# Kernel tuning notes

Measured on AMD Instinct MI355X. Metric: run time of the kernel, lower is better.

The kernel has to match this reference:

```python
import jax, jax.numpy as jnp
from jax import lax
import numpy as np

B, S, H, E = 512, 128, 512, 128
VEC_FEAT = 128
WORD_VOCABS = [1000, 500, 200]
GOAL_VOCAB = 32000
TACTIC_VOCAB = 1024
NUM_ENC_LAYERS = 3  # -> 2 extra encoder linear layers


def setup_inputs() -> dict:
    key = jax.random.key(0)
    ks = iter(jax.random.split(key, 32))
    s = 0.05
    inp = {}
    inp["vec_features"] = jax.random.normal(next(ks), (B, VEC_FEAT), dtype=jnp.float32)
    inp["word_features"] = jax.random.randint(next(ks), (B, len(WORD_VOCABS)), 0, 200)
    inp["goals"] = jax.random.randint(next(ks), (B, S), 0, GOAL_VOCAB)
    # word feature embedding tables (distinct vocab sizes)
    inp["wemb0"] = jax.random.normal(next(ks), (WORD_VOCABS[0], E), dtype=jnp.float32) * s
    inp["wemb1"] = jax.random.normal(next(ks), (WORD_VOCABS[1], E), dtype=jnp.float32) * s
    inp["wemb2"] = jax.random.normal(next(ks), (WORD_VOCABS[2], E), dtype=jnp.float32) * s
    # features_in: Linear(vec_feat + 3*E -> H), torch convention W [out, in]
    inp["feat_in_W"] = jax.random.normal(next(ks), (H, VEC_FEAT + len(WORD_VOCABS) * E), dtype=jnp.float32) * s
    inp["feat_in_b"] = jnp.zeros((H,), dtype=jnp.float32)
    # stacked encoder layers: (L-1) x Linear(H -> H)
    inp["enc_W"] = jax.random.normal(next(ks), (NUM_ENC_LAYERS - 1, H, H), dtype=jnp.float32) * s
    inp["enc_b"] = jnp.zeros((NUM_ENC_LAYERS - 1, H), dtype=jnp.float32)
    inp["goal_emb"] = jax.random.normal(next(ks), (GOAL_VOCAB, H), dtype=jnp.float32) * s
    # GRU weights, torch layout: [3H, H] with gate order (r, z, n)
    inp["gru_Wih"] = jax.random.normal(next(ks), (3 * H, H), dtype=jnp.float32) * s
    inp["gru_Whh"] = jax.random.normal(next(ks), (3 * H, H), dtype=jnp.float32) * s
    inp["gru_bih"] = jnp.zeros((3 * H,), dtype=jnp.float32)
    inp["gru_bhh"] = jnp.zeros((3 * H,), dtype=jnp.float32)
    inp["dec_in_W"] = jax.random.normal(next(ks), (H, 2 * H), dtype=jnp.float32) * s
    inp["dec_in_b"] = jnp.zeros((H,), dtype=jnp.float32)
    inp["dec_out_W"] = jax.random.normal(next(ks), (TACTIC_VOCAB, H), dtype=jnp.float32) * s
    inp["dec_out_b"] = jnp.zeros((TACTIC_VOCAB,), dtype=jnp.float32)
    return inp


def reference(vec_features, word_features, goals, wemb0, wemb1, wemb2,
              feat_in_W, feat_in_b, enc_W, enc_b, goal_emb,
              gru_Wih, gru_Whh, gru_bih, gru_bhh,
              dec_in_W, dec_in_b, dec_out_W, dec_out_b):
    batch = vec_features.shape[0]
    h = gru_Whh.shape[1]
    # Goal GRU branch: relu(embedding) per token, then GRU recurrence.
    x_seq = jax.nn.relu(goal_emb[goals])                    # [B, S, H]
    # Precompute input-side gate projections for all timesteps: [B, S, 3H]
    gi = jnp.einsum('bsh,gh->bsg', x_seq, gru_Wih) + gru_bih

    def step(hid, gi_t):
        gh = hid @ gru_Whh.T + gru_bhh                      # [B, 3H]
        i_r, i_z, i_n = jnp.split(gi_t, 3, axis=-1)
        h_r, h_z, h_n = jnp.split(gh, 3, axis=-1)
        r = jax.nn.sigmoid(i_r + h_r)
        z = jax.nn.sigmoid(i_z + h_z)
        n = jnp.tanh(i_n + r * h_n)
        new = (1.0 - z) * n + z * hid
        return new, None

    h0 = jnp.zeros((batch, h), dtype=x_seq.dtype)
    goal_data, _ = lax.scan(step, h0, jnp.swapaxes(gi, 0, 1))  # [B, H]

    # Features branch: word-feature embeddings + vec features -> MLP
    embs = [wemb0[word_features[:, 0]], wemb1[word_features[:, 1]], wemb2[word_features[:, 2]]]
    feats = jnp.concatenate([vec_features] + embs, axis=1)
    features_data = feats @ feat_in_W.T + feat_in_b
    for i in range(enc_W.shape[0]):
        features_data = jax.nn.relu(features_data) @ enc_W[i].T + enc_b[i]

    full = jax.nn.relu(jnp.concatenate([goal_data, features_data], axis=1))
    full = jax.nn.relu(full @ dec_in_W.T + dec_in_b)
    logits = full @ dec_out_W.T + dec_out_b
    return jax.nn.log_softmax(logits, axis=1)
```

## Files before the change

### kernel.cpp

```cpp
#include <hip/hip_runtime.h>
#include <hip/hip_bf16.h>

typedef unsigned short ushort_t;
typedef __attribute__((ext_vector_type(8))) short short8;
typedef __attribute__((ext_vector_type(4))) float f32x4;
typedef __attribute__((ext_vector_type(4))) int i32x4;

__device__ __forceinline__ ushort_t f2bf(float f) {
    unsigned x = __builtin_bit_cast(unsigned, f);
    unsigned r = x + 0x7fffu + ((x >> 16) & 1u);
    return (ushort_t)(r >> 16);
}
__device__ __forceinline__ float bf2f(ushort_t u) {
    return __builtin_bit_cast(float, ((unsigned)u) << 16);
}

__device__ __forceinline__ void store16_cc(void* p, i32x4 v) {
    asm volatile("global_store_dwordx4 %0, %1, off sc0 sc1" :: "v"(p), "v"(v) : "memory");
}
__device__ __forceinline__ i32x4 load16_cc(const void* p) {
    i32x4 r;
    asm volatile("global_load_dwordx4 %0, %1, off sc0 sc1" : "=v"(r) : "v"(p));
    return r;
}
__device__ __forceinline__ unsigned load_u16_raw(const ushort_t* p) {
    unsigned r;
    asm volatile("global_load_ushort %0, %1, off" : "=v"(r) : "v"(p));
    return r;
}

template<bool RELU>
__global__ void k_conv(const float* __restrict__ src, ushort_t* __restrict__ dst, int n) {
    int i = (blockIdx.x * blockDim.x + threadIdx.x) * 4;
    int stride = gridDim.x * blockDim.x * 4;
    for (; i < n; i += stride) {
        float4 v = *(const float4*)(src + i);
        if (RELU) {
            v.x = fmaxf(v.x, 0.f); v.y = fmaxf(v.y, 0.f);
            v.z = fmaxf(v.z, 0.f); v.w = fmaxf(v.w, 0.f);
        }
        dst[i + 0] = f2bf(v.x); dst[i + 1] = f2bf(v.y);
        dst[i + 2] = f2bf(v.z); dst[i + 3] = f2bf(v.w);
    }
}

__global__ void k_whh_frag(const float* __restrict__ whh, ushort_t* __restrict__ out) {
    int idx = blockIdx.x * blockDim.x + threadIdx.x;
    if (idx >= 16 * 6 * 16 * 64 * 8) return;
    int e  = idx & 7;
    int s  = idx >> 3;
    int l  = s & 63;
    int s2 = s >> 6;
    int kk = s2 & 15;
    int s3 = s2 >> 4;
    int f  = s3 % 6;
    int j  = s3 / 6;
    int ng = (f >> 1) * 512 + j * 32 + (f & 1) * 16 + (l & 15);
    int k  = kk * 32 + ((l >> 4) << 3) + e;
    out[idx] = f2bf(whh[(size_t)ng * 512 + k]);
}

__global__ void k_feats(const float* __restrict__ vec, const int* __restrict__ wf,
                        const float* __restrict__ w0, const float* __restrict__ w1,
                        const float* __restrict__ w2, ushort_t* __restrict__ out) {
    int idx = blockIdx.x * blockDim.x + threadIdx.x;
    if (idx >= 512 * 512) return;
    int b = idx >> 9, k = idx & 511;
    float v;
    if (k < 128)       v = vec[b * 128 + k];
    else if (k < 256)  v = w0[wf[b * 3 + 0] * 128 + (k - 128)];
    else if (k < 384)  v = w1[wf[b * 3 + 1] * 128 + (k - 256)];
    else               v = w2[wf[b * 3 + 2] * 128 + (k - 384)];
    out[idx] = f2bf(v);
}

template<bool RELU, bool OUTBF>
__global__ __launch_bounds__(256) void k_gemm(const ushort_t* __restrict__ A,
                                              const ushort_t* __restrict__ W,
                                              const float* __restrict__ bias,
                                              void* __restrict__ Cout,
                                              int M, int N, int K) {
    __shared__ __attribute__((aligned(16))) ushort_t As[128 * 64];
    __shared__ __attribute__((aligned(16))) ushort_t Ws[128 * 64];
    const int tid = threadIdx.x;
    const int lane = tid & 63, w = tid >> 6;
    const int wm = w >> 1, wn = w & 1;
    const int m0 = blockIdx.y * 128, n0 = blockIdx.x * 128;
    const int l16 = lane & 15, lq = lane >> 4;
    f32x4 acc[4][4] = {};

    for (int k0 = 0; k0 < K; k0 += 64) {
        #pragma unroll
        for (int c = 0; c < 4; ++c) {
            int chunk = w * 4 + c;
            int d = chunk * 1024 + lane * 16;
            int row = d >> 7;
            int dlin = d ^ ((row & 7) << 4);
            int col = (dlin & 127) >> 1;
            const ushort_t* ga = A + (size_t)(m0 + row) * K + k0 + col;
            __builtin_amdgcn_global_load_lds(
                (const __attribute__((address_space(1))) void*)ga,
                (__attribute__((address_space(3))) void*)(((char*)As) + chunk * 1024),
                16, 0, 0);
        }
        #pragma unroll
        for (int c = 0; c < 4; ++c) {
            int chunk = w * 4 + c;
            int d = chunk * 1024 + lane * 16;
            int row = d >> 7;
            int dlin = d ^ ((row & 7) << 4);
            int col = (dlin & 127) >> 1;
            const ushort_t* gw = W + (size_t)(n0 + row) * K + k0 + col;
            __builtin_amdgcn_global_load_lds(
                (const __attribute__((address_space(1))) void*)gw,
                (__attribute__((address_space(3))) void*)(((char*)Ws) + chunk * 1024),
                16, 0, 0);
        }
        asm volatile("s_waitcnt vmcnt(0)" ::: "memory");
        __syncthreads();

        #pragma unroll
        for (int kk = 0; kk < 2; ++kk) {
            short8 af[4], bfr[4];
            #pragma unroll
            for (int m = 0; m < 4; ++m) {
                int row = wm * 64 + m * 16 + l16;
                int addr = (row * 128 + kk * 64 + lq * 16) ^ ((row & 7) << 4);
                af[m] = *(const short8*)((const char*)As + addr);
            }
            #pragma unroll
            for (int n = 0; n < 4; ++n) {
                int row = wn * 64 + n * 16 + l16;
                int addr = (row * 128 + kk * 64 + lq * 16) ^ ((row & 7) << 4);
                bfr[n] = *(const short8*)((const char*)Ws + addr);
            }
            #pragma unroll
            for (int m = 0; m < 4; ++m)
                #pragma unroll
                for (int n = 0; n < 4; ++n)
                    acc[m][n] = __builtin_amdgcn_mfma_f32_16x16x32_bf16(af[m], bfr[n], acc[m][n], 0, 0, 0);
        }
        __syncthreads();
    }

    #pragma unroll
    for (int m = 0; m < 4; ++m) {
        int row = m0 + wm * 64 + m * 16 + lq * 4;
        #pragma unroll
        for (int n = 0; n < 4; ++n) {
            int col = n0 + wn * 64 + n * 16 + l16;
            float bv = bias[col];
            #pragma unroll
            for (int r = 0; r < 4; ++r) {
                float v = acc[m][n][r] + bv;
                if (RELU) v = fmaxf(v, 0.f);
                if (OUTBF) ((ushort_t*)Cout)[(size_t)(row + r) * N + col] = f2bf(v);
                else       ((float*)Cout)[(size_t)(row + r) * N + col] = v;
            }
        }
    }
}

__global__ __launch_bounds__(128) void k_recur(const ushort_t* __restrict__ G,
                                               const ushort_t* __restrict__ WhhF,
                                               const int* __restrict__ goals,
                                               const float* __restrict__ bhh,
                                               ushort_t* __restrict__ Hx,
                                               int* __restrict__ flags,
                                               float* __restrict__ goal_out) {
    __shared__ __attribute__((aligned(16))) ushort_t Bs[6 * 16 * 64 * 8];
    __shared__ __attribute__((aligned(16))) ushort_t Hs[32 * 32];
    __shared__ __attribute__((aligned(16))) int Tk[32 * 128];
    const int bid = blockIdx.x;
    const int rg = bid & 15;
    const int cg = bid >> 4;
    const int r0 = rg * 32, c0 = cg * 32;
    const int tid = threadIdx.x, lane = tid & 63, w = tid >> 6;
    const int l16 = lane & 15, lq = lane >> 4;

    {
        const ushort_t* src = WhhF + (size_t)cg * 49152;
        for (int c = 0; c < 48; ++c) {
            int chunk = w * 48 + c;
            __builtin_amdgcn_global_load_lds(
                (const __attribute__((address_space(1))) void*)(src + chunk * 512 + lane * 8),
                (__attribute__((address_space(3))) void*)(((char*)Bs) + chunk * 1024),
                16, 0, 0);
        }
        const int* tsrc = goals + r0 * 128;
        for (int c = 0; c < 8; ++c) {
            int chunk = w * 8 + c;
            __builtin_amdgcn_global_load_lds(
                (const __attribute__((address_space(1))) void*)(tsrc + chunk * 256 + lane * 4),
                (__attribute__((address_space(3))) void*)(((char*)Tk) + chunk * 1024),
                16, 0, 0);
        }
        asm volatile("s_waitcnt vmcnt(0)" ::: "memory");
        __syncthreads();
    }

    const int rowbase = r0 + w * 16;
    const int lrow = w * 16 + lq * 4;
    float hst[2][4];
    #pragma unroll
    for (int q = 0; q < 2; ++q)
        #pragma unroll
        for (int r = 0; r < 4; ++r) hst[q][r] = 0.f;

    float bh[3][2];
    #pragma unroll
    for (int g = 0; g < 3; ++g)
        #pragma unroll
        for (int q = 0; q < 2; ++q) bh[g][q] = bhh[g * 512 + c0 + q * 16 + l16];

    float gc[3][4][2];
    #pragma unroll
    for (int r = 0; r < 4; ++r) {
        int tok = Tk[(lrow + r) * 128];
        const ushort_t* gr = G + (size_t)tok * 1536;
        #pragma unroll
        for (int q = 0; q < 2; ++q) {
            int cl = c0 + q * 16 + l16;
            gc[0][r][q] = bf2f(gr[cl]);
            gc[1][r][q] = bf2f(gr[512 + cl]);
            gc[2][r][q] = bf2f(gr[1024 + cl]);
        }
    }

    unsigned gn[3][4][2];
    auto issueGN = [&](int tn) {
        #pragma unroll
        for (int r = 0; r < 4; ++r) {
            int tok = Tk[(lrow + r) * 128 + tn];
            const ushort_t* gr = G + (size_t)tok * 1536;
            #pragma unroll
            for (int q = 0; q < 2; ++q) {
                int cl = c0 + q * 16 + l16;
                gn[0][r][q] = load_u16_raw(gr + cl);
                gn[1][r][q] = load_u16_raw(gr + 512 + cl);
                gn[2][r][q] = load_u16_raw(gr + 1024 + cl);
            }
        }
    };

    for (int t = 0; t < 128; ++t) {
        const int tn = (t < 127) ? t + 1 : 127;
        f32x4 acc[6] = {};
        if (t) {
            const ushort_t* hb = Hx + ((size_t)(t & 1) << 18);
            short8 af[16];
            #pragma unroll
            for (int kk = 0; kk < 16; ++kk) {
                const ushort_t* pa = hb + (size_t)(rowbase + l16) * 512 + kk * 32 + lq * 8;
                af[kk] = __builtin_bit_cast(short8, load16_cc(pa));
            }
            issueGN(tn);
            asm volatile("s_waitcnt vmcnt(24)" ::: "memory");
            __builtin_amdgcn_sched_barrier(0);
            #pragma unroll
            for (int kk = 0; kk < 16; ++kk) {
                #pragma unroll
                for (int f = 0; f < 6; ++f) {
                    short8 bfr = *(const short8*)((const char*)Bs + ((f * 16 + kk) * 64 + lane) * 16);
                    acc[f] = __builtin_amdgcn_mfma_f32_16x16x32_bf16(af[kk], bfr, acc[f], 0, 0, 0);
                }
            }
        } else {
            issueGN(tn);
        }

        #pragma unroll
        for (int r = 0; r < 4; ++r) {
            #pragma unroll
            for (int q = 0; q < 2; ++q) {
                float ir = gc[0][r][q], iz = gc[1][r][q], in_ = gc[2][r][q];
                float hr = acc[q][r] + bh[0][q];
                float hz = acc[2 + q][r] + bh[1][q];
                float hn = acc[4 + q][r] + bh[2][q];
                float rr = 1.f / (1.f + __expf(-(ir + hr)));
                float zz = 1.f / (1.f + __expf(-(iz + hz)));
                float x = in_ + rr * hn;
                float ax = fabsf(x);
                float th = 1.f - 2.f / (__expf(2.f * ax) + 1.f);
                th = copysignf(th, x);
                float hnew = (1.f - zz) * th + zz * hst[q][r];
                hst[q][r] = hnew;
                Hs[(w * 16 + lq * 4 + r) * 32 + q * 16 + l16] = f2bf(hnew);
            }
        }
        __syncthreads();

        {
            int row = tid >> 2, coff = (tid & 3) * 8;
            i32x4 v = *(const i32x4*)&Hs[row * 32 + coff];
            ushort_t* ho = Hx + ((size_t)((t + 1) & 1) << 18)
                         + (size_t)(r0 + row) * 512 + c0 + coff;
            store16_cc(ho, v);
        }
        asm volatile("s_waitcnt vmcnt(0)" ::: "memory");
        __builtin_amdgcn_sched_barrier(0);
        __syncthreads();

        if (tid == 0)
            __hip_atomic_store(&flags[bid], t + 1, __ATOMIC_RELAXED, __HIP_MEMORY_SCOPE_AGENT);
        if (tid < 16) {
            int* pf = &flags[(tid << 4) | rg];
            for (int it = 0; it < 100000; ++it) {
                if (__hip_atomic_load(pf, __ATOMIC_RELAXED, __HIP_MEMORY_SCOPE_AGENT) >= t + 1)
                    break;
                __builtin_amdgcn_s_sleep(1);
            }
        }
        __syncthreads();

        #pragma unroll
        for (int g = 0; g < 3; ++g)
            #pragma unroll
            for (int r = 0; r < 4; ++r)
                #pragma unroll
                for (int q = 0; q < 2; ++q)
                    gc[g][r][q] = bf2f((ushort_t)gn[g][r][q]);
    }

    #pragma unroll
    for (int r = 0; r < 4; ++r) {
        int brow = rowbase + lq * 4 + r;
        #pragma unroll
        for (int q = 0; q < 2; ++q) {
            int cl = c0 + q * 16 + l16;
            goal_out[(size_t)brow * 512 + cl] = hst[q][r];
        }
    }
}

__global__ void k_concat(const float* __restrict__ gd, const ushort_t* __restrict__ r2,
                         ushort_t* __restrict__ out) {
    int idx = blockIdx.x * blockDim.x + threadIdx.x;
    if (idx >= 512 * 1024) return;
    int b = idx >> 10, c = idx & 1023;
    out[idx] = (c < 512) ? f2bf(fmaxf(gd[b * 512 + c], 0.f)) : r2[b * 512 + (c - 512)];
}

__global__ __launch_bounds__(256) void k_lsm(float* __restrict__ logits) {
    __shared__ float sm[4];
    __shared__ float ss[4];
    float* p = logits + (size_t)blockIdx.x * 1024;
    int tid = threadIdx.x;
    float4 v = ((const float4*)p)[tid];
    float m = fmaxf(fmaxf(v.x, v.y), fmaxf(v.z, v.w));
    #pragma unroll
    for (int o = 32; o >= 1; o >>= 1) m = fmaxf(m, __shfl_xor(m, o));
    if ((tid & 63) == 0) sm[tid >> 6] = m;
    __syncthreads();
    m = fmaxf(fmaxf(sm[0], sm[1]), fmaxf(sm[2], sm[3]));
    float s = __expf(v.x - m) + __expf(v.y - m) + __expf(v.z - m) + __expf(v.w - m);
    #pragma unroll
    for (int o = 32; o >= 1; o >>= 1) s += __shfl_xor(s, o);
    if ((tid & 63) == 0) ss[tid >> 6] = s;
    __syncthreads();
    s = ss[0] + ss[1] + ss[2] + ss[3];
    float lse = m + logf(s);
    v.x -= lse; v.y -= lse; v.z -= lse; v.w -= lse;
    ((float4*)p)[tid] = v;
}

static constexpr size_t OFF_G     = 0;
static constexpr size_t OFF_AREL  = OFF_G     + 98304000ull;
static constexpr size_t OFF_WIH   = OFF_AREL  + 32768000ull;
static constexpr size_t OFF_WHHF  = OFF_WIH   + 1572864ull;
static constexpr size_t OFF_HX    = OFF_WHHF  + 1572864ull;
static constexpr size_t OFF_FLAGS = OFF_HX    + 1048576ull;
static constexpr size_t OFF_GOAL  = OFF_FLAGS + 1024ull;
static constexpr size_t OFF_FEATS = OFF_GOAL  + 1048576ull;
static constexpr size_t OFF_W0    = OFF_FEATS + 524288ull;
static constexpr size_t OFF_W12   = OFF_W0    + 524288ull;
static constexpr size_t OFF_R0    = OFF_W12   + 1048576ull;
static constexpr size_t OFF_R1    = OFF_R0    + 524288ull;
static constexpr size_t OFF_R2    = OFF_R1    + 524288ull;
static constexpr size_t OFF_DECA  = OFF_R2    + 524288ull;
static constexpr size_t OFF_WD1   = OFF_DECA  + 1048576ull;
static constexpr size_t OFF_D1    = OFF_WD1   + 1048576ull;
static constexpr size_t OFF_WD2   = OFF_D1    + 524288ull;
static constexpr size_t WS_NEED   = OFF_WD2   + 1048576ull;

extern "C" void kernel_launch(void* const* d_in, const int* in_sizes, int n_in,
                              void* d_out, int out_size, void* d_ws, size_t ws_size,
                              hipStream_t stream) {
    if (ws_size < WS_NEED) return;

    const float* vec   = (const float*)d_in[0];
    const int*   wf    = (const int*)d_in[1];
    const int*   goals = (const int*)d_in[2];
    const float* we0   = (const float*)d_in[3];
    const float* we1   = (const float*)d_in[4];
    const float* we2   = (const float*)d_in[5];
    const float* fiW   = (const float*)d_in[6];
    const float* fib   = (const float*)d_in[7];
    const float* encW  = (const float*)d_in[8];
    const float* encb  = (const float*)d_in[9];
    const float* gemb  = (const float*)d_in[10];
    const float* Wih   = (const float*)d_in[11];
    const float* Whh   = (const float*)d_in[12];
    const float* bih   = (const float*)d_in[13];
    const float* bhh   = (const float*)d_in[14];
    const float* diW   = (const float*)d_in[15];
    const float* dib   = (const float*)d_in[16];
    const float* doW   = (const float*)d_in[17];
    const float* dob   = (const float*)d_in[18];

    char* ws = (char*)d_ws;
    ushort_t* G_     = (ushort_t*)(ws + OFF_G);
    ushort_t* Arel   = (ushort_t*)(ws + OFF_AREL);
    ushort_t* WihB   = (ushort_t*)(ws + OFF_WIH);
    ushort_t* WhhF   = (ushort_t*)(ws + OFF_WHHF);
    ushort_t* Hx     = (ushort_t*)(ws + OFF_HX);
    int*      flags  = (int*)(ws + OFF_FLAGS);
    float*    goalD  = (float*)(ws + OFF_GOAL);
    ushort_t* featsA = (ushort_t*)(ws + OFF_FEATS);
    ushort_t* W0     = (ushort_t*)(ws + OFF_W0);
    ushort_t* W1     = (ushort_t*)(ws + OFF_W12);
    ushort_t* W2     = W1 + 262144;
    ushort_t* R0     = (ushort_t*)(ws + OFF_R0);
    ushort_t* R1     = (ushort_t*)(ws + OFF_R1);
    ushort_t* R2     = (ushort_t*)(ws + OFF_R2);
    ushort_t* DecA   = (ushort_t*)(ws + OFF_DECA);
    ushort_t* Wd1    = (ushort_t*)(ws + OFF_WD1);
    ushort_t* D1     = (ushort_t*)(ws + OFF_D1);
    ushort_t* Wd2    = (ushort_t*)(ws + OFF_WD2);

    hipMemsetAsync(ws + OFF_FLAGS, 0, 1024, stream);

    auto cgrid = [](int n) { int b = (n / 4 + 255) / 256; return b > 2048 ? 2048 : b; };
    k_conv<false><<<cgrid(786432),  256, 0, stream>>>(Wih,  WihB, 786432);
    k_conv<false><<<cgrid(262144),  256, 0, stream>>>(fiW,  W0,   262144);
    k_conv<false><<<cgrid(524288),  256, 0, stream>>>(encW, W1,   524288);
    k_conv<false><<<cgrid(524288),  256, 0, stream>>>(diW,  Wd1,  524288);
    k_conv<false><<<cgrid(524288),  256, 0, stream>>>(doW,  Wd2,  524288);
    k_conv<true ><<<2048,           256, 0, stream>>>(gemb, Arel, 16384000);
    k_whh_frag<<<3072, 256, 0, stream>>>(Whh, WhhF);
    k_feats<<<1024, 256, 0, stream>>>(vec, wf, we0, we1, we2, featsA);

    k_gemm<false, true><<<dim3(12, 250), 256, 0, stream>>>(Arel, WihB, bih, G_, 32000, 1536, 512);

    k_gemm<true, true><<<dim3(4, 4), 256, 0, stream>>>(featsA, W0, fib,        R0, 512, 512, 512);
    k_gemm<true, true><<<dim3(4, 4), 256, 0, stream>>>(R0,     W1, encb,       R1, 512, 512, 512);
    k_gemm<true, true><<<dim3(4, 4), 256, 0, stream>>>(R1,     W2, encb + 512, R2, 512, 512, 512);

    {
        const ushort_t* Gc = G_; const ushort_t* Wc = WhhF;
        const int* gc = goals; const float* bc = bhh;
        ushort_t* hx = Hx; int* fl = flags; float* go = goalD;
        void* kargs[] = { &Gc, &Wc, &gc, &bc, &hx, &fl, &go };
        hipLaunchCooperativeKernel((const void*)k_recur, dim3(256), dim3(128),
                                   kargs, 0, stream);
    }

    k_concat<<<2048, 256, 0, stream>>>(goalD, R2, DecA);
    k_gemm<true,  true ><<<dim3(4, 4), 256, 0, stream>>>(DecA, Wd1, dib, D1, 512, 512, 1024);
    k_gemm<false, false><<<dim3(8, 4), 256, 0, stream>>>(D1, Wd2, dob, (float*)d_out, 512, 1024, 512);
    k_lsm<<<512, 256, 0, stream>>>((float*)d_out);
}
```

Baseline: 1.173 ms.

## Replace block-wide flag barrier with per-chunk readiness polling in GRU recurrence

The persistent GRU kernel no longer waits for all 16 peer blocks to publish their hidden-state slice before each step. Each wave starts with its own slice from LDS, then polls the peer flags and loads and multiplies each 32-column chunk as soon as its producer has signalled, double-buffering the A fragments. One __syncthreads per step is also dropped, and the gate-input prefetch is reissued at the end of each step rather than kept in a separate register copy. This targets the grid-wide barrier cost on the sequential recurrence, at the price of frequent uncached flag loads, more control flow, and correctness that depends on memory ordering between the flag store and the data store.

```diff
diff --git a/kernel.cpp b/kernel.cpp
--- a/kernel.cpp
+++ b/kernel.cpp
@@ -213,22 +213,8 @@
         #pragma unroll
         for (int q = 0; q < 2; ++q) bh[g][q] = bhh[g * 512 + c0 + q * 16 + l16];
 
-    float gc[3][4][2];
-    #pragma unroll
-    for (int r = 0; r < 4; ++r) {
-        int tok = Tk[(lrow + r) * 128];
-        const ushort_t* gr = G + (size_t)tok * 1536;
-        #pragma unroll
-        for (int q = 0; q < 2; ++q) {
-            int cl = c0 + q * 16 + l16;
-            gc[0][r][q] = bf2f(gr[cl]);
-            gc[1][r][q] = bf2f(gr[512 + cl]);
-            gc[2][r][q] = bf2f(gr[1024 + cl]);
-        }
-    }
-
-    unsigned gn[3][4][2];
-    auto issueGN = [&](int tn) {
+    unsigned gv[3][4][2];
+    auto issueGV = [&](int tn) {
         #pragma unroll
         for (int r = 0; r < 4; ++r) {
             int tok = Tk[(lrow + r) * 128 + tn];
@@ -236,44 +222,83 @@
             #pragma unroll
             for (int q = 0; q < 2; ++q) {
                 int cl = c0 + q * 16 + l16;
-                gn[0][r][q] = load_u16_raw(gr + cl);
-                gn[1][r][q] = load_u16_raw(gr + 512 + cl);
-                gn[2][r][q] = load_u16_raw(gr + 1024 + cl);
+                gv[0][r][q] = load_u16_raw(gr + cl);
+                gv[1][r][q] = load_u16_raw(gr + 512 + cl);
+                gv[2][r][q] = load_u16_raw(gr + 1024 + cl);
             }
         }
     };
-
+    issueGV(0);
+
+    int* fp = flags + (((lane & 15) << 4) | rg);
+
+    f32x4 acc[6];
     for (int t = 0; t < 128; ++t) {
-        const int tn = (t < 127) ? t + 1 : 127;
-        f32x4 acc[6] = {};
+        #pragma unroll
+        for (int f = 0; f < 6; ++f) acc[f] = (f32x4){0.f, 0.f, 0.f, 0.f};
+
+        auto domfma = [&](short8 af, int kk) {
+            #pragma unroll
+            for (int f = 0; f < 6; ++f) {
+                short8 bfr = *(const short8*)((const char*)Bs + ((f * 16 + kk) * 64 + lane) * 16);
+                acc[f] = __builtin_amdgcn_mfma_f32_16x16x32_bf16(af, bfr, acc[f], 0, 0, 0);
+            }
+        };
+        auto pollrdy = [&]() -> unsigned {
+            int v;
+            asm volatile("global_load_dword %0, %1, off sc0 sc1" : "=v"(v) : "v"(fp));
+            asm volatile("s_waitcnt vmcnt(0)" ::: "memory");
+            __builtin_amdgcn_sched_barrier(0);
+            return (unsigned)(__ballot(v >= t) & 0xffffull);
+        };
+
         if (t) {
             const ushort_t* hb = Hx + ((size_t)(t & 1) << 18);
-            short8 af[16];
-            #pragma unroll
-            for (int kk = 0; kk < 16; ++kk) {
-                const ushort_t* pa = hb + (size_t)(rowbase + l16) * 512 + kk * 32 + lq * 8;
-                af[kk] = __builtin_bit_cast(short8, load16_cc(pa));
-            }
-            issueGN(tn);
-            asm volatile("s_waitcnt vmcnt(24)" ::: "memory");
+            auto tadr = [&](int j) {
+                return hb + (size_t)(rowbase + l16) * 512 + j * 32 + lq * 8;
+            };
+            short8 own = *(const short8*)&Hs[(w * 16 + l16) * 32 + lq * 8];
+            domfma(own, cg);
+            unsigned rdy = pollrdy();
+            short8 afr[2];
+            {
+                int j1 = (cg + 1) & 15;
+                int guard = 0;
+                while (!((rdy >> j1) & 1)) {
+                    rdy = pollrdy();
+                    if (++guard > 200000) break;
+                }
+                afr[1] = __builtin_bit_cast(short8, load16_cc(tadr(j1)));
+            }
+            #pragma unroll
+            for (int s = 1; s <= 15; ++s) {
+                if (s < 15) {
+                    int jn = (cg + s + 1) & 15;
+                    int guard = 0;
+                    while (!((rdy >> jn) & 1)) {
+                        rdy = pollrdy();
+                        if (++guard > 200000) break;
+                    }
+                    afr[(s + 1) & 1] = __builtin_bit_cast(short8, load16_cc(tadr(jn)));
+                    asm volatile("s_waitcnt vmcnt(1)" ::: "memory");
+                } else {
+                    asm volatile("s_waitcnt vmcnt(0)" ::: "memory");
+                }
+                __builtin_amdgcn_sched_barrier(0);
+                domfma(afr[s & 1], (cg + s) & 15);
+            }
+        } else {
+            asm volatile("s_waitcnt vmcnt(0)" ::: "memory");
             __builtin_amdgcn_sched_barrier(0);
-            #pragma unroll
-            for (int kk = 0; kk < 16; ++kk) {
-                #pragma unroll
-                for (int f = 0; f < 6; ++f) {
-                    short8 bfr = *(const short8*)((const char*)Bs + ((f * 16 + kk) * 64 + lane) * 16);
-                    acc[f] = __builtin_amdgcn_mfma_f32_16x16x32_bf16(af[kk], bfr, acc[f], 0, 0, 0);
-                }
-            }
-        } else {
-            issueGN(tn);
         }
 
         #pragma unroll
         for (int r = 0; r < 4; ++r) {
             #pragma unroll
             for (int q = 0; q < 2; ++q) {
-                float ir = gc[0][r][q], iz = gc[1][r][q], in_ = gc[2][r][q];
+                float ir = bf2f((ushort_t)gv[0][r][q]);
+                float iz = bf2f((ushort_t)gv[1][r][q]);
+                float in_ = bf2f((ushort_t)gv[2][r][q]);
                 float hr = acc[q][r] + bh[0][q];
                 float hz = acc[2 + q][r] + bh[1][q];
                 float hn = acc[4 + q][r] + bh[2][q];
@@ -288,7 +313,6 @@
                 Hs[(w * 16 + lq * 4 + r) * 32 + q * 16 + l16] = f2bf(hnew);
             }
         }
-        __syncthreads();
 
         {
             int row = tid >> 2, coff = (tid & 3) * 8;
@@ -301,25 +325,12 @@
         __builtin_amdgcn_sched_barrier(0);
         __syncthreads();
 
-        if (tid == 0)
-            __hip_atomic_store(&flags[bid], t + 1, __ATOMIC_RELAXED, __HIP_MEMORY_SCOPE_AGENT);
-        if (tid < 16) {
-            int* pf = &flags[(tid << 4) | rg];
-            for (int it = 0; it < 100000; ++it) {
-                if (__hip_atomic_load(pf, __ATOMIC_RELAXED, __HIP_MEMORY_SCOPE_AGENT) >= t + 1)
-                    break;
-                __builtin_amdgcn_s_sleep(1);
-            }
-        }
-        __syncthreads();
-
-        #pragma unroll
-        for (int g = 0; g < 3; ++g)
-            #pragma unroll
-            for (int r = 0; r < 4; ++r)
-                #pragma unroll
-                for (int q = 0; q < 2; ++q)
-                    gc[g][r][q] = bf2f((ushort_t)gn[g][r][q]);
+        if (tid == 0) {
+            int fvv = t + 1;
+            asm volatile("global_store_dword %0, %1, off sc0 sc1"
+                         :: "v"(&flags[bid]), "v"(fvv) : "memory");
+        }
+        issueGV(t < 127 ? t + 1 : 127);
     }
 
     #pragma unroll
```

New measurement: 1.002 ms. 14.5% less time.
